# Optimization experiments

Hardware: AMD Instinct MI355X
Metric: run time of the kernel (lower is better)

## Reference

```python
import jax, jax.numpy as jnp
import numpy as np

# --- static module config (from init_kwargs) ---
C1_OUT = 64          # c1OutChannels
C1K = 400            # k winners in conv layer
N_FC = 1024          # fc1 hidden units (n)
K_FC = 100           # k winners in fc1
BOOST = 1.0          # boostStrength
W_SPARSITY = 0.5     # weightSparsity: fraction of fc1 weights allowed nonzero
HP = 12              # pooled spatial size: floor((28-5+1)/2)
C1_OUTPUT_LEN = C1_OUT * HP * HP  # 9216
BATCH = 4096


def setup_inputs() -> dict:
    key = jax.random.key(0)
    ks = jax.random.split(key, 10)
    x = jax.random.normal(ks[0], (BATCH, 1, 28, 28), jnp.float32)
    c1_w = jax.random.normal(ks[1], (C1_OUT, 1, 5, 5), jnp.float32) * 0.1
    c1_b = jax.random.normal(ks[2], (C1_OUT,), jnp.float32) * 0.01
    # duty cycles live in [0, ~density]
    duty_cnn = jax.random.uniform(ks[3], (1, C1_OUT, 1, 1), jnp.float32) * 0.05
    fc1_w = jax.random.normal(ks[4], (N_FC, C1_OUT_LEN_ := C1_OUTPUT_LEN), jnp.float32) * 0.01
    fc1_mask_raw = jax.random.uniform(ks[5], (N_FC, C1_OUTPUT_LEN), jnp.float32)
    fc1_b = jax.random.normal(ks[6], (N_FC,), jnp.float32) * 0.01
    duty_fc = jax.random.uniform(ks[7], (N_FC,), jnp.float32) * 0.1
    fc2_w = jax.random.normal(ks[8], (10, N_FC), jnp.float32) * 0.05
    fc2_b = jnp.zeros((10,), jnp.float32)
    return dict(x=x, c1_w=c1_w, c1_b=c1_b, duty_cnn=duty_cnn, fc1_w=fc1_w,
                fc1_mask_raw=fc1_mask_raw, fc1_b=fc1_b, duty_fc=duty_fc,
                fc2_w=fc2_w, fc2_b=fc2_b)


def _kwinners(x_flat, boost_flat, k):
    """Duty-cycle-boosted k-winner mask.
    x_flat: [B, N]; boost_flat: [1, N] broadcastable boost factors.
    Keeps original x values at the top-k boosted positions per row, zeros rest.
    Boosting uses stop_gradient(x), matching KWinners*.forward(x.detach()*boost).
    """
    boosted = jax.lax.stop_gradient(x_flat) * boost_flat
    thr = jax.lax.top_k(boosted, k)[0][:, -1:]  # k-th largest per row
    return jnp.where(boosted >= thr, x_flat, jnp.zeros((), x_flat.dtype))


def reference(x, c1_w, c1_b, duty_cnn, fc1_w, fc1_mask_raw, fc1_b, duty_fc,
              fc2_w, fc2_b):
    B = x.shape[0]
    # conv2d (valid, stride 1) -> [B, 64, 24, 24]
    y = jax.lax.conv_general_dilated(
        x, c1_w, window_strides=(1, 1), padding='VALID',
        dimension_numbers=('NCHW', 'OIHW', 'NCHW')) + c1_b[None, :, None, None]
    # max_pool2d(2) -> [B, 64, 12, 12]
    y = jax.lax.reduce_window(y, -jnp.inf, jax.lax.max,
                              (1, 1, 2, 2), (1, 1, 2, 2), 'VALID')
    # KWinnersCNN: global top-k over flattened (C,H,W), per-channel boost
    target_density = C1K / C1_OUTPUT_LEN
    boost_c = jnp.exp((target_density - duty_cnn) * BOOST)  # [1,C,1,1]
    boost_flat = jnp.broadcast_to(boost_c, (1, C1_OUT, HP, HP)).reshape(1, -1)
    yf = _kwinners(y.reshape(B, -1), boost_flat, C1K)  # [B, 9216]
    # LinearSDR fc1: sparse-weight linear + KWinners
    w_mask = (fc1_mask_raw < W_SPARSITY).astype(fc1_w.dtype)
    h = yf @ (fc1_w * w_mask).T + fc1_b  # [B, 1024]
    boost_fc = jnp.exp((K_FC / N_FC - duty_fc) * BOOST)[None, :]
    h = _kwinners(h, boost_fc, K_FC)
    # fc2 + log_softmax (dropout inactive in eval mode)
    logits = h @ fc2_w.T + fc2_b
    return jax.nn.log_softmax(logits, axis=1)
```

## Files before the change

kernel.cpp:

```cpp
#include <hip/hip_runtime.h>

__device__ __forceinline__ float b2f(unsigned short u) {
  return __uint_as_float(((unsigned)u) << 16);
}
__device__ __forceinline__ unsigned short f2b(float f) {
  unsigned u = __float_as_uint(f);
  return (unsigned short)((u + 0x7FFFu + ((u >> 16) & 1u)) >> 16);
}
__device__ __forceinline__ float gload(const void* p, int i, int isb) {
  return isb ? b2f(((const unsigned short*)p)[i]) : ((const float*)p)[i];
}
__device__ __forceinline__ unsigned tokey(float f) {
  unsigned u = __float_as_uint(f);
  return u ^ (unsigned)(((int)u >> 31) | 0x80000000u);
}

__global__ void k_detect(const void* x, int* flag) {
  int tid = threadIdx.x;
  unsigned short u = ((const unsigned short*)x)[2 * tid];
  int e = (u >> 7) & 0xFF;
  bool sane = (e >= 100 && e <= 140);
  unsigned long long m = __ballot(sane);
  if (tid == 0) *flag = (__popcll(m) >= 40) ? 1 : 0;
}

__global__ __launch_bounds__(256) void k_prep(const void* __restrict__ fc1w,
                                              const void* __restrict__ mraw,
                                              float* __restrict__ WtF,
                                              const int* __restrict__ flag) {
  __shared__ float tile[64][65];
  const int isb = *flag;
  const int i0 = blockIdx.x * 64;
  const int u0 = blockIdx.y * 64;
  const int tx = threadIdx.x & 63, ty = threadIdx.x >> 6;
  for (int uu = ty; uu < 64; uu += 4) {
    int gi = (u0 + uu) * 9216 + i0 + tx;
    float wv = gload(fc1w, gi, isb);
    float mv = gload(mraw, gi, isb);
    tile[uu][tx] = (mv < 0.5f) ? wv : 0.0f;
  }
  __syncthreads();
  for (int ii = ty; ii < 64; ii += 4)
    WtF[(i0 + ii) * 1024 + u0 + tx] = tile[tx][ii];
}

__global__ __launch_bounds__(256) void k_conv(const void* __restrict__ x,
                                              const void* __restrict__ c1w_g,
                                              const void* __restrict__ c1b_g,
                                              const void* __restrict__ duty_g,
                                              int2* __restrict__ wpair,
                                              int* __restrict__ wcnt,
                                              const int* __restrict__ flag) {
  __shared__ __align__(16) float img[784];
  __shared__ float cw[1600];
  __shared__ float cb[64], bcs[64];
  __shared__ __align__(16) float pooled[9216];
  __shared__ unsigned hist4[4][256];
  __shared__ unsigned wtot[4];
  __shared__ unsigned selb, selk;
  const int tid = threadIdx.x;
  const int b = blockIdx.x;
  const int isb = *flag;
  const int lane = tid & 63;
  const int wv_id = tid >> 6;

  for (int i = tid; i < 784; i += 256) img[i] = gload(x, b * 784 + i, isb);
  for (int i = tid; i < 1600; i += 256) cw[i] = gload(c1w_g, i, isb);
  if (tid < 64) {
    cb[tid] = gload(c1b_g, tid, isb);
    float arg = (float)(400.0 / 9216.0) - gload(duty_g, tid, isb);
    bcs[tid] = (float)exp((double)arg);
  }
  __syncthreads();

  {
    const int c = tid >> 2;
    const int half = tid & 1;
    const int ph0 = ((tid >> 1) & 1) * 6;
    float w[25];
#pragma unroll
    for (int i = 0; i < 25; ++i) w[i] = cw[c * 25 + i];
    const float bias = cb[c];
    float R[6][16];
#pragma unroll
    for (int r = 0; r < 6; ++r) {
      int ir = 2 * ph0 + r;
#pragma unroll
      for (int q = 0; q < 4; ++q)
        ((float4*)&R[r][0])[q] = ((const float4*)img)[ir * 7 + half * 3 + q];
    }
#pragma unroll
    for (int i = 0; i < 6; ++i) {
      const int ph = ph0 + i;
      float a0[12], a1[12];
#pragma unroll
      for (int j = 0; j < 12; ++j) { a0[j] = 0.f; a1[j] = 0.f; }
#pragma unroll
      for (int kj = 0; kj < 5; ++kj) {
#pragma unroll
        for (int kr = 0; kr < 5; ++kr) {
          float wk = w[kr * 5 + kj];
          const float* r0 = &R[(2 * i + kr) % 6][0];
          const float* r1 = &R[(2 * i + kr + 1) % 6][0];
#pragma unroll
          for (int j = 0; j < 12; ++j) {
            a0[j] = fmaf(r0[j + kj], wk, a0[j]);
            a1[j] = fmaf(r1[j + kj], wk, a1[j]);
          }
        }
      }
      int obase = c * 144 + ph * 12 + half * 6;
#pragma unroll
      for (int q = 0; q < 6; ++q) {
        float m = fmaxf(fmaxf(a0[2 * q], a0[2 * q + 1]),
                        fmaxf(a1[2 * q], a1[2 * q + 1]));
        pooled[obase + q] = m + bias;
      }
      if (i < 5) {
        int ir0 = 2 * ph + 6, ir1 = 2 * ph + 7;
        float* d0 = &R[(2 * i) % 6][0];
        float* d1 = &R[(2 * i + 1) % 6][0];
#pragma unroll
        for (int q = 0; q < 4; ++q) {
          ((float4*)d0)[q] = ((const float4*)img)[ir0 * 7 + half * 3 + q];
          ((float4*)d1)[q] = ((const float4*)img)[ir1 * 7 + half * 3 + q];
        }
      }
    }
  }
  __syncthreads();

  unsigned keys[36];
  {
    const float bcf = bcs[tid >> 2];
#pragma unroll
    for (int e4 = 0; e4 < 9; ++e4) {
      float4 pv = ((float4*)pooled)[tid * 9 + e4];
      keys[4 * e4 + 0] = tokey(pv.x * bcf);
      keys[4 * e4 + 1] = tokey(pv.y * bcf);
      keys[4 * e4 + 2] = tokey(pv.z * bcf);
      keys[4 * e4 + 3] = tokey(pv.w * bcf);
    }
  }

  unsigned kfix = 0;
  unsigned kk = 400;
  for (int pass = 3; pass >= 0; --pass) {
    const int shift = pass * 8;
    const unsigned himask = (pass == 3) ? 0u : (0xFFFFFFFFu << (shift + 8));
#pragma unroll
    for (int w2 = 0; w2 < 4; ++w2) hist4[w2][tid] = 0;
    __syncthreads();
    unsigned* myh = hist4[wv_id];
#pragma unroll
    for (int e = 0; e < 36; ++e) {
      unsigned key = keys[e];
      if (((key ^ kfix) & himask) == 0)
        atomicAdd(&myh[(key >> shift) & 255u], 1u);
    }
    __syncthreads();
    unsigned own = hist4[0][tid] + hist4[1][tid] + hist4[2][tid] + hist4[3][tid];
    unsigned v = own;
#pragma unroll
    for (int off = 1; off < 64; off <<= 1) {
      unsigned y = __shfl_down(v, off, 64);
      if (lane + off < 64) v += y;
    }
    if (lane == 0) wtot[wv_id] = v;
    __syncthreads();
#pragma unroll
    for (int w2 = 0; w2 < 4; ++w2)
      if (w2 > wv_id) v += wtot[w2];
    unsigned snext = v - own;
    if (v >= kk && snext < kk) {
      selb = (unsigned)tid;
      selk = kk - snext;
    }
    __syncthreads();
    kfix |= selb << shift;
    kk = selk;
    __syncthreads();
  }

  unsigned mycnt = 0;
#pragma unroll
  for (int e = 0; e < 36; ++e) mycnt += (keys[e] >= kfix) ? 1u : 0u;
  unsigned px = mycnt;
#pragma unroll
  for (int off = 1; off < 64; off <<= 1) {
    unsigned y = __shfl_up(px, off, 64);
    if (lane >= off) px += y;
  }
  if (lane == 63) wtot[wv_id] = px;
  __syncthreads();
  unsigned base = 0;
#pragma unroll
  for (int w2 = 0; w2 < 4; ++w2)
    if (w2 < wv_id) base += wtot[w2];
  int pos = (int)(base + px - mycnt);
  for (int e = 0; e < 36; ++e) {
    if (keys[e] >= kfix) {
      int o = tid * 36 + e;
      if (pos < 512)
        wpair[b * 512 + pos] = make_int2(__float_as_int(pooled[o]), o << 12);
      ++pos;
    }
  }
  if (tid == 0) {
    unsigned tot = wtot[0] + wtot[1] + wtot[2] + wtot[3];
    wcnt[b] = (int)(tot < 512u ? tot : 512u);
  }
}

__global__ __launch_bounds__(128) void k_fc1(const float* __restrict__ WtF,
                                             const int2* __restrict__ wpair,
                                             const int* __restrict__ wcnt,
                                             const void* __restrict__ fc1b,
                                             float* __restrict__ h,
                                             const int* __restrict__ flag,
                                             int img_base) {
  __shared__ __align__(16) int2 wl[512];
  const int tid = threadIdx.x;
  const int img = img_base + (blockIdx.x >> 3);
  const int slice = blockIdx.x & 7;
  const int isb = *flag;
  const int cnt = wcnt[img];
  const int2* __restrict__ wp = wpair + img * 512;
  for (int i = tid; i < cnt; i += 128) wl[i] = wp[i];
  __syncthreads();
  const int u = (slice << 7) + tid;
  const char* __restrict__ Wb = (const char*)WtF + (unsigned)u * 4u;
  const int4* wl4 = (const int4*)wl;
  float acc = 0.f;
  int w = 0;
  for (; w + 8 <= cnt; w += 8) {
    const int b4 = w >> 1;
    int4 q0 = wl4[b4 + 0];
    int4 q1 = wl4[b4 + 1];
    int4 q2 = wl4[b4 + 2];
    int4 q3 = wl4[b4 + 3];
    acc = fmaf(__int_as_float(q0.x), *(const float*)(Wb + (unsigned)q0.y), acc);
    acc = fmaf(__int_as_float(q0.z), *(const float*)(Wb + (unsigned)q0.w), acc);
    acc = fmaf(__int_as_float(q1.x), *(const float*)(Wb + (unsigned)q1.y), acc);
    acc = fmaf(__int_as_float(q1.z), *(const float*)(Wb + (unsigned)q1.w), acc);
    acc = fmaf(__int_as_float(q2.x), *(const float*)(Wb + (unsigned)q2.y), acc);
    acc = fmaf(__int_as_float(q2.z), *(const float*)(Wb + (unsigned)q2.w), acc);
    acc = fmaf(__int_as_float(q3.x), *(const float*)(Wb + (unsigned)q3.y), acc);
    acc = fmaf(__int_as_float(q3.z), *(const float*)(Wb + (unsigned)q3.w), acc);
  }
  for (; w < cnt; ++w) {
    int2 p = wl[w];
    acc = fmaf(__int_as_float(p.x), *(const float*)(Wb + (unsigned)p.y), acc);
  }
  h[img * 1024 + u] = acc + gload(fc1b, u, isb);
}

__global__ __launch_bounds__(256) void k_boost(const void* __restrict__ dutyfc,
                                               float* __restrict__ bf,
                                               const int* __restrict__ flag) {
  const int u = blockIdx.x * 256 + threadIdx.x;
  const int isb = *flag;
  if (u < 1024)
    bf[u] = (float)exp((double)(0.09765625f - gload(dutyfc, u, isb)));
}

__global__ __launch_bounds__(256) void k_sel(const float* __restrict__ h,
                                             const float* __restrict__ bf,
                                             const void* __restrict__ fc2w,
                                             const void* __restrict__ fc2b,
                                             void* __restrict__ out,
                                             const int* __restrict__ flag) {
  __shared__ unsigned hist4[4][256];
  __shared__ unsigned wtot[4];
  __shared__ unsigned selb, selk;
  __shared__ double lg[10];
  __shared__ double mred[2];
  const int tid = threadIdx.x;
  const int row = blockIdx.x;
  const int isb = *flag;
  const int lane = tid & 63;
  const int wv_id = tid >> 6;
  if (tid < 10) lg[tid] = (double)gload(fc2b, tid, isb);
  __syncthreads();

  const int u0 = 2 * tid, u1 = 2 * tid + 1, u2 = 512 + 2 * tid, u3 = 513 + 2 * tid;
  float2 hlo = ((const float2*)(h + row * 1024))[tid];
  float2 hhi = ((const float2*)(h + row * 1024 + 512))[tid];
  float h0 = hlo.x, h1 = hlo.y, h2 = hhi.x, h3 = hhi.y;
  float2 blo = ((const float2*)bf)[tid];
  float2 bhi = ((const float2*)(bf + 512))[tid];
  unsigned k0 = tokey(h0 * blo.x);
  unsigned k1 = tokey(h1 * blo.y);
  unsigned k2 = tokey(h2 * bhi.x);
  unsigned k3 = tokey(h3 * bhi.y);

  unsigned kfix = 0;
  unsigned kk = 100;
  for (int pass = 3; pass >= 0; --pass) {
    const int shift = pass * 8;
    const unsigned himask = (pass == 3) ? 0u : (0xFFFFFFFFu << (shift + 8));
#pragma unroll
    for (int w2 = 0; w2 < 4; ++w2) hist4[w2][tid] = 0;
    __syncthreads();
    unsigned* myh = hist4[wv_id];
    if (((k0 ^ kfix) & himask) == 0) atomicAdd(&myh[(k0 >> shift) & 255u], 1u);
    if (((k1 ^ kfix) & himask) == 0) atomicAdd(&myh[(k1 >> shift) & 255u], 1u);
    if (((k2 ^ kfix) & himask) == 0) atomicAdd(&myh[(k2 >> shift) & 255u], 1u);
    if (((k3 ^ kfix) & himask) == 0) atomicAdd(&myh[(k3 >> shift) & 255u], 1u);
    __syncthreads();
    unsigned own = hist4[0][tid] + hist4[1][tid] + hist4[2][tid] + hist4[3][tid];
    unsigned v = own;
#pragma unroll
    for (int off = 1; off < 64; off <<= 1) {
      unsigned y = __shfl_down(v, off, 64);
      if (lane + off < 64) v += y;
    }
    if (lane == 0) wtot[wv_id] = v;
    __syncthreads();
#pragma unroll
    for (int w2 = 0; w2 < 4; ++w2)
      if (w2 > wv_id) v += wtot[w2];
    unsigned snext = v - own;
    if (v >= kk && snext < kk) {
      selb = (unsigned)tid;
      selk = kk - snext;
    }
    __syncthreads();
    kfix |= selb << shift;
    kk = selk;
    __syncthreads();
  }
  bool kp0 = k0 >= kfix, kp1 = k1 >= kfix, kp2 = k2 >= kfix, kp3 = k3 >= kfix;

  double part[10];
#pragma unroll
  for (int c = 0; c < 10; ++c) part[c] = 0.0;
  if (kp0) {
#pragma unroll
    for (int c = 0; c < 10; ++c) part[c] = fma((double)h0, (double)gload(fc2w, c * 1024 + u0, isb), part[c]);
  }
  if (kp1) {
#pragma unroll
    for (int c = 0; c < 10; ++c) part[c] = fma((double)h1, (double)gload(fc2w, c * 1024 + u1, isb), part[c]);
  }
  if (kp2) {
#pragma unroll
    for (int c = 0; c < 10; ++c) part[c] = fma((double)h2, (double)gload(fc2w, c * 1024 + u2, isb), part[c]);
  }
  if (kp3) {
#pragma unroll
    for (int c = 0; c < 10; ++c) part[c] = fma((double)h3, (double)gload(fc2w, c * 1024 + u3, isb), part[c]);
  }
#pragma unroll
  for (int c = 0; c < 10; ++c) {
    double p = part[c];
    for (int off = 32; off > 0; off >>= 1) p += __shfl_xor(p, off);
    if ((tid & 63) == 0) atomicAdd(&lg[c], p);
  }
  __syncthreads();
  if (tid == 0) {
    double m = lg[0];
#pragma unroll
    for (int c = 1; c < 10; ++c) m = lg[c] > m ? lg[c] : m;
    double sum = 0.0;
#pragma unroll
    for (int c = 0; c < 10; ++c) sum += exp(lg[c] - m);
    mred[0] = m;
    mred[1] = log(sum);
  }
  __syncthreads();
  if (tid < 10) {
    double o = lg[tid] - mred[0] - mred[1];
    if (isb)
      ((unsigned short*)out)[row * 10 + tid] = f2b((float)o);
    else
      ((float*)out)[row * 10 + tid] = (float)o;
  }
}

extern "C" void kernel_launch(void* const* d_in, const int* in_sizes, int n_in,
                              void* d_out, int out_size, void* d_ws, size_t ws_size,
                              hipStream_t stream) {
  char* ws = (char*)d_ws;
  float* WtF = (float*)ws;
  int2* wpair = (int2*)(ws + 37748736);
  int* wcnt = (int*)(ws + 54525952);
  float* h = (float*)(ws + 54542336);
  int* flag = (int*)(ws + 71319552);
  float* bf = WtF;

  k_detect<<<1, 64, 0, stream>>>(d_in[0], flag);
  k_prep<<<dim3(144, 16), 256, 0, stream>>>(d_in[4], d_in[5], WtF, flag);
  k_conv<<<4096, 256, 0, stream>>>(d_in[0], d_in[1], d_in[2], d_in[3],
                                   wpair, wcnt, flag);
  k_fc1<<<2048 * 8, 128, 0, stream>>>(WtF, wpair, wcnt, d_in[6], h, flag, 0);
  k_fc1<<<2048 * 8, 128, 0, stream>>>(WtF, wpair, wcnt, d_in[6], h, flag, 2048);
  k_boost<<<4, 256, 0, stream>>>(d_in[7], bf, flag);
  k_sel<<<4096, 256, 0, stream>>>(h, bf, d_in[8], d_in[9], d_out, flag);
}
```

Baseline: 627.0 us.

## Add fp32-specialized conv/top-k kernel reading image from global, smaller shared memory

Adds a float32-only conv+pool+kwinners kernel that reads the image and conv weights straight from global memory instead of staging them in shared memory. It also halves the histogram shared array from four copies to two. This cuts per-block LDS use, which should allow more resident blocks, and drops the bf16 branching in the hot loop. The original kernel now exits early for fp32 inputs, so both kernels launch every call. The cost is an extra kernel launch plus more atomic contention on the shared histograms.

Measured after the change: 696.1 us. +11.0%, slower.

```diff
diff --git a/kernel.cpp b/kernel.cpp
--- a/kernel.cpp
+++ b/kernel.cpp
@@ -44,6 +44,193 @@
     WtF[(i0 + ii) * 1024 + u0 + tx] = tile[tx][ii];
 }
 
+__global__ __launch_bounds__(256) void k_convf(const float* __restrict__ x,
+                                               const float* __restrict__ c1w,
+                                               const float* __restrict__ c1b,
+                                               const float* __restrict__ duty,
+                                               int2* __restrict__ wpair,
+                                               int* __restrict__ wcnt,
+                                               const int* __restrict__ flag) {
+  if (*flag) return;
+  __shared__ __align__(16) float pooled[9216];
+  __shared__ unsigned hist2[2][256];
+  __shared__ float cb[64], bcs[64];
+  __shared__ unsigned wtot[4];
+  __shared__ unsigned selb, selk;
+  const int tid = threadIdx.x;
+  const int b = blockIdx.x;
+  const int lane = tid & 63;
+  const int wv_id = tid >> 6;
+
+  if (tid < 64) {
+    cb[tid] = c1b[tid];
+    float arg = (float)(400.0 / 9216.0) - duty[tid];
+    bcs[tid] = (float)exp((double)arg);
+  }
+  __syncthreads();
+
+  {
+    const float* __restrict__ imgg = x + b * 784;
+    const int c = tid >> 2;
+    const int half = tid & 1;
+    const int ph0 = ((tid >> 1) & 1) * 6;
+    float w[25];
+#pragma unroll
+    for (int i = 0; i < 25; ++i) w[i] = c1w[c * 25 + i];
+    const float bias = cb[c];
+    float R[6][16];
+#pragma unroll
+    for (int r = 0; r < 6; ++r) {
+      int ir = 2 * ph0 + r;
+#pragma unroll
+      for (int q = 0; q < 4; ++q)
+        ((float4*)&R[r][0])[q] = ((const float4*)imgg)[ir * 7 + half * 3 + q];
+    }
+#pragma unroll
+    for (int i = 0; i < 6; ++i) {
+      const int ph = ph0 + i;
+      float a0[12], a1[12];
+#pragma unroll
+      for (int j = 0; j < 12; ++j) { a0[j] = 0.f; a1[j] = 0.f; }
+#pragma unroll
+      for (int kj = 0; kj < 5; ++kj) {
+#pragma unroll
+        for (int kr = 0; kr < 5; ++kr) {
+          float wk = w[kr * 5 + kj];
+          const float* r0 = &R[(2 * i + kr) % 6][0];
+          const float* r1 = &R[(2 * i + kr + 1) % 6][0];
+#pragma unroll
+          for (int j = 0; j < 12; ++j) {
+            a0[j] = fmaf(r0[j + kj], wk, a0[j]);
+            a1[j] = fmaf(r1[j + kj], wk, a1[j]);
+          }
+        }
+      }
+      int obase = c * 144 + ph * 12 + half * 6;
+#pragma unroll
+      for (int q = 0; q < 6; ++q) {
+        float m = fmaxf(fmaxf(a0[2 * q], a0[2 * q + 1]),
+                        fmaxf(a1[2 * q], a1[2 * q + 1]));
+        pooled[obase + q] = m + bias;
+      }
+      if (i < 5) {
+        int ir0 = 2 * ph + 6, ir1 = 2 * ph + 7;
+        float* d0 = &R[(2 * i) % 6][0];
+        float* d1 = &R[(2 * i + 1) % 6][0];
+#pragma unroll
+        for (int q = 0; q < 4; ++q) {
+          ((float4*)d0)[q] = ((const float4*)imgg)[ir0 * 7 + half * 3 + q];
+          ((float4*)d1)[q] = ((const float4*)imgg)[ir1 * 7 + half * 3 + q];
+        }
+      }
+    }
+  }
+  __syncthreads();
+
+  unsigned keys[36];
+  {
+    const float bcf = bcs[tid >> 2];
+#pragma unroll
+    for (int e4 = 0; e4 < 9; ++e4) {
+      float4 pv = ((float4*)pooled)[tid * 9 + e4];
+      keys[4 * e4 + 0] = tokey(pv.x * bcf);
+      keys[4 * e4 + 1] = tokey(pv.y * bcf);
+      keys[4 * e4 + 2] = tokey(pv.z * bcf);
+      keys[4 * e4 + 3] = tokey(pv.w * bcf);
+    }
+  }
+
+  unsigned kfix = 0;
+  unsigned kk = 400;
+  unsigned long long cand = 0xFFFFFFFFFFFFFFFFull >> 28;
+  for (int pass = 3; pass >= 0; --pass) {
+    const int shift = pass * 8;
+    const unsigned himask = (pass == 3) ? 0u : (0xFFFFFFFFu << (shift + 8));
+    hist2[0][tid] = 0;
+    hist2[1][tid] = 0;
+    __syncthreads();
+    unsigned* myh = hist2[wv_id >> 1];
+    if (pass == 3) {
+      unsigned cbin = 0xFFFFFFFFu, ccnt = 0;
+#pragma unroll
+      for (int e = 0; e < 36; ++e) {
+        unsigned bin = keys[e] >> 24;
+        if (bin == cbin) {
+          ++ccnt;
+        } else {
+          if (ccnt) atomicAdd(&myh[cbin], ccnt);
+          cbin = bin;
+          ccnt = 1;
+        }
+      }
+      if (ccnt) atomicAdd(&myh[cbin], ccnt);
+    } else {
+      unsigned long long m = cand;
+      unsigned long long keep = 0;
+      while (m) {
+        int e = __builtin_ctzll(m);
+        m &= m - 1;
+        if (((keys[e] ^ kfix) & himask) == 0) {
+          atomicAdd(&myh[(keys[e] >> shift) & 255u], 1u);
+          keep |= 1ull << e;
+        }
+      }
+      cand = keep;
+    }
+    __syncthreads();
+    unsigned own = hist2[0][tid] + hist2[1][tid];
+    unsigned v = own;
+#pragma unroll
+    for (int off = 1; off < 64; off <<= 1) {
+      unsigned y = __shfl_down(v, off, 64);
+      if (lane + off < 64) v += y;
+    }
+    if (lane == 0) wtot[wv_id] = v;
+    __syncthreads();
+#pragma unroll
+    for (int w2 = 0; w2 < 4; ++w2)
+      if (w2 > wv_id) v += wtot[w2];
+    unsigned snext = v - own;
+    if (v >= kk && snext < kk) {
+      selb = (unsigned)tid;
+      selk = kk - snext;
+    }
+    __syncthreads();
+    kfix |= selb << shift;
+    kk = selk;
+    __syncthreads();
+  }
+
+  unsigned mycnt = 0;
+#pragma unroll
+  for (int e = 0; e < 36; ++e) mycnt += (keys[e] >= kfix) ? 1u : 0u;
+  unsigned px = mycnt;
+#pragma unroll
+  for (int off = 1; off < 64; off <<= 1) {
+    unsigned y = __shfl_up(px, off, 64);
+    if (lane >= off) px += y;
+  }
+  if (lane == 63) wtot[wv_id] = px;
+  __syncthreads();
+  unsigned base = 0;
+#pragma unroll
+  for (int w2 = 0; w2 < 4; ++w2)
+    if (w2 < wv_id) base += wtot[w2];
+  int pos = (int)(base + px - mycnt);
+  for (int e = 0; e < 36; ++e) {
+    if (keys[e] >= kfix) {
+      int o = tid * 36 + e;
+      if (pos < 512)
+        wpair[b * 512 + pos] = make_int2(__float_as_int(pooled[o]), o << 12);
+      ++pos;
+    }
+  }
+  if (tid == 0) {
+    unsigned tot = wtot[0] + wtot[1] + wtot[2] + wtot[3];
+    wcnt[b] = (int)(tot < 512u ? tot : 512u);
+  }
+}
+
 __global__ __launch_bounds__(256) void k_conv(const void* __restrict__ x,
                                               const void* __restrict__ c1w_g,
                                               const void* __restrict__ c1b_g,
@@ -51,6 +238,8 @@
                                               int2* __restrict__ wpair,
                                               int* __restrict__ wcnt,
                                               const int* __restrict__ flag) {
+  const int isb = *flag;
+  if (!isb) return;
   __shared__ __align__(16) float img[784];
   __shared__ float cw[1600];
   __shared__ float cb[64], bcs[64];
@@ -60,7 +249,6 @@
   __shared__ unsigned selb, selk;
   const int tid = threadIdx.x;
   const int b = blockIdx.x;
-  const int isb = *flag;
   const int lane = tid & 63;
   const int wv_id = tid >> 6;
 
@@ -391,6 +579,9 @@
 
   k_detect<<<1, 64, 0, stream>>>(d_in[0], flag);
   k_prep<<<dim3(144, 16), 256, 0, stream>>>(d_in[4], d_in[5], WtF, flag);
+  k_convf<<<4096, 256, 0, stream>>>((const float*)d_in[0], (const float*)d_in[1],
+                                    (const float*)d_in[2], (const float*)d_in[3],
+                                    wpair, wcnt, flag);
   k_conv<<<4096, 256, 0, stream>>>(d_in[0], d_in[1], d_in[2], d_in[3],
                                    wpair, wcnt, flag);
   k_fc1<<<2048 * 8, 128, 0, stream>>>(WtF, wpair, wcnt, d_in[6], h, flag, 0);
```

## Process two images per fc1 block with float2 weight gathers per lane

Applied to the files above, without the earlier changes.

Each 128-thread fc1 block now handles two images, one per wavefront. Each lane computes two adjacent output units using float2 weight gathers, so every winner index loads 8 bytes instead of 4 and grid size is halved. The aim is fewer gather instructions and better use of each memory transaction on the transposed weight matrix. In exchange, per-wave work rises and the number of wavefronts covering each image slice drops, which may reduce latency hiding.

Result: slower. 732.9 us (+16.9%).

```diff
diff --git a/kernel.cpp b/kernel.cpp
--- a/kernel.cpp
+++ b/kernel.cpp
@@ -218,20 +218,23 @@
                                              const void* __restrict__ fc1b,
                                              float* __restrict__ h,
                                              const int* __restrict__ flag,
-                                             int img_base) {
-  __shared__ __align__(16) int2 wl[512];
+                                             int pair_base) {
+  __shared__ __align__(16) int2 wl[1024];
   const int tid = threadIdx.x;
-  const int img = img_base + (blockIdx.x >> 3);
+  const int lane = tid & 63;
+  const int wv = tid >> 6;
+  const int img = (pair_base + (int)(blockIdx.x >> 3)) * 2 + wv;
   const int slice = blockIdx.x & 7;
   const int isb = *flag;
   const int cnt = wcnt[img];
   const int2* __restrict__ wp = wpair + img * 512;
-  for (int i = tid; i < cnt; i += 128) wl[i] = wp[i];
-  __syncthreads();
-  const int u = (slice << 7) + tid;
+  int2* mywl = wl + (wv << 9);
+  for (int i = lane; i < cnt; i += 64) mywl[i] = wp[i];
+  __syncthreads();
+  const int u = (slice << 7) + (lane << 1);
   const char* __restrict__ Wb = (const char*)WtF + (unsigned)u * 4u;
-  const int4* wl4 = (const int4*)wl;
-  float acc = 0.f;
+  const int4* wl4 = (const int4*)mywl;
+  float acc0 = 0.f, acc1 = 0.f;
   int w = 0;
   for (; w + 8 <= cnt; w += 8) {
     const int b4 = w >> 1;
@@ -239,20 +242,41 @@
     int4 q1 = wl4[b4 + 1];
     int4 q2 = wl4[b4 + 2];
     int4 q3 = wl4[b4 + 3];
-    acc = fmaf(__int_as_float(q0.x), *(const float*)(Wb + (unsigned)q0.y), acc);
-    acc = fmaf(__int_as_float(q0.z), *(const float*)(Wb + (unsigned)q0.w), acc);
-    acc = fmaf(__int_as_float(q1.x), *(const float*)(Wb + (unsigned)q1.y), acc);
-    acc = fmaf(__int_as_float(q1.z), *(const float*)(Wb + (unsigned)q1.w), acc);
-    acc = fmaf(__int_as_float(q2.x), *(const float*)(Wb + (unsigned)q2.y), acc);
-    acc = fmaf(__int_as_float(q2.z), *(const float*)(Wb + (unsigned)q2.w), acc);
-    acc = fmaf(__int_as_float(q3.x), *(const float*)(Wb + (unsigned)q3.y), acc);
-    acc = fmaf(__int_as_float(q3.z), *(const float*)(Wb + (unsigned)q3.w), acc);
+    float2 m0 = *(const float2*)(Wb + (unsigned)q0.y);
+    float2 m1 = *(const float2*)(Wb + (unsigned)q0.w);
+    float2 m2 = *(const float2*)(Wb + (unsigned)q1.y);
+    float2 m3 = *(const float2*)(Wb + (unsigned)q1.w);
+    float2 m4 = *(const float2*)(Wb + (unsigned)q2.y);
+    float2 m5 = *(const float2*)(Wb + (unsigned)q2.w);
+    float2 m6 = *(const float2*)(Wb + (unsigned)q3.y);
+    float2 m7 = *(const float2*)(Wb + (unsigned)q3.w);
+    acc0 = fmaf(__int_as_float(q0.x), m0.x, acc0);
+    acc1 = fmaf(__int_as_float(q0.x), m0.y, acc1);
+    acc0 = fmaf(__int_as_float(q0.z), m1.x, acc0);
+    acc1 = fmaf(__int_as_float(q0.z), m1.y, acc1);
+    acc0 = fmaf(__int_as_float(q1.x), m2.x, acc0);
+    acc1 = fmaf(__int_as_float(q1.x), m2.y, acc1);
+    acc0 = fmaf(__int_as_float(q1.z), m3.x, acc0);
+    acc1 = fmaf(__int_as_float(q1.z), m3.y, acc1);
+    acc0 = fmaf(__int_as_float(q2.x), m4.x, acc0);
+    acc1 = fmaf(__int_as_float(q2.x), m4.y, acc1);
+    acc0 = fmaf(__int_as_float(q2.z), m5.x, acc0);
+    acc1 = fmaf(__int_as_float(q2.z), m5.y, acc1);
+    acc0 = fmaf(__int_as_float(q3.x), m6.x, acc0);
+    acc1 = fmaf(__int_as_float(q3.x), m6.y, acc1);
+    acc0 = fmaf(__int_as_float(q3.z), m7.x, acc0);
+    acc1 = fmaf(__int_as_float(q3.z), m7.y, acc1);
   }
   for (; w < cnt; ++w) {
-    int2 p = wl[w];
-    acc = fmaf(__int_as_float(p.x), *(const float*)(Wb + (unsigned)p.y), acc);
-  }
-  h[img * 1024 + u] = acc + gload(fc1b, u, isb);
+    int2 p = mywl[w];
+    float2 m = *(const float2*)(Wb + (unsigned)p.y);
+    acc0 = fmaf(__int_as_float(p.x), m.x, acc0);
+    acc1 = fmaf(__int_as_float(p.x), m.y, acc1);
+  }
+  float2 o;
+  o.x = acc0 + gload(fc1b, u, isb);
+  o.y = acc1 + gload(fc1b, u + 1, isb);
+  *(float2*)(h + img * 1024 + u) = o;
 }
 
 __global__ __launch_bounds__(256) void k_boost(const void* __restrict__ dutyfc,
@@ -393,8 +417,8 @@
   k_prep<<<dim3(144, 16), 256, 0, stream>>>(d_in[4], d_in[5], WtF, flag);
   k_conv<<<4096, 256, 0, stream>>>(d_in[0], d_in[1], d_in[2], d_in[3],
                                    wpair, wcnt, flag);
-  k_fc1<<<2048 * 8, 128, 0, stream>>>(WtF, wpair, wcnt, d_in[6], h, flag, 0);
-  k_fc1<<<2048 * 8, 128, 0, stream>>>(WtF, wpair, wcnt, d_in[6], h, flag, 2048);
+  k_fc1<<<1024 * 8, 128, 0, stream>>>(WtF, wpair, wcnt, d_in[6], h, flag, 0);
+  k_fc1<<<1024 * 8, 128, 0, stream>>>(WtF, wpair, wcnt, d_in[6], h, flag, 1024);
   k_boost<<<4, 256, 0, stream>>>(d_in[7], bf, flag);
   k_sel<<<4096, 256, 0, stream>>>(h, bf, d_in[8], d_in[9], d_out, flag);
 }
```
